# Optimization experiments

Measured on AMD Instinct MI355X. Metric: run time of the kernel, lower is better.

## Reference

```python
import jax, jax.numpy as jnp
import numpy as np


def setup_inputs() -> dict:
    key = jax.random.key(0)
    k1, k2, k3, k4, k5 = jax.random.split(key, 5)
    B, S, IN, OUT = 4, 2048, 4096, 11008
    x = jax.random.normal(k1, (B, S, IN), dtype=jnp.float32)
    # uint8-style codes stored as int32 (per-channel int8 WOQ)
    qweight = jax.random.randint(k2, (OUT, IN), 0, 256, dtype=jnp.int32)
    scales = jax.random.uniform(k3, (OUT,), dtype=jnp.float32) * 0.01 + 1e-4
    zero_points = jax.random.uniform(k4, (OUT,), dtype=jnp.float32) * 255.0
    bias = jax.random.normal(k5, (OUT,), dtype=jnp.float32)
    return {"x": x, "qweight": qweight, "scales": scales,
            "zero_points": zero_points, "bias": bias}


def reference(x, qweight, scales, zero_points, bias):
    # Inline dequantization of per-output-channel quantized weight:
    # W[o, i] = (q[o, i] - zp[o]) * scale[o]
    w = (qweight.astype(jnp.float32) - zero_points[:, None]) * scales[:, None]
    # Y = x @ W^T + b  -> [B, S, OUT]
    y = jnp.einsum("bsi,oi->bso", x, w) + bias
    return y
```

## Files before the change

kernel.cpp:

```cpp
#include <hip/hip_runtime.h>
#include <stdint.h>

#define MDIM 8192
#define NDIM 11008
#define KDIM 4096
#define BM 128
#define BN 128
#define BK 32

typedef __bf16 bf16x8 __attribute__((ext_vector_type(8)));
typedef float floatx4 __attribute__((ext_vector_type(4)));

typedef const __attribute__((address_space(1))) void* gas_ptr;
typedef __attribute__((address_space(3))) void* las_ptr;

__device__ __forceinline__ unsigned short f32_bf16_rne(float f) {
    union { float f; unsigned u; } v; v.f = f;
    unsigned r = 0x7FFFu + ((v.u >> 16) & 1u);
    return (unsigned short)((v.u + r) >> 16);
}

__global__ __launch_bounds__(256) void convert_x_kernel(
    const float* __restrict__ x, unsigned short* __restrict__ xb)
{
    const size_t gid = (size_t)blockIdx.x * 256 + threadIdx.x;
    const float4* p = (const float4*)x + gid * 2;
    float4 a = p[0], b = p[1];
    unsigned short t[8];
    t[0] = f32_bf16_rne(a.x); t[1] = f32_bf16_rne(a.y);
    t[2] = f32_bf16_rne(a.z); t[3] = f32_bf16_rne(a.w);
    t[4] = f32_bf16_rne(b.x); t[5] = f32_bf16_rne(b.y);
    t[6] = f32_bf16_rne(b.z); t[7] = f32_bf16_rne(b.w);
    *(uint4*)(xb + gid * 8) = *(const uint4*)t;
}

__global__ __launch_bounds__(256) void dequant_w_kernel(
    const int* __restrict__ q, const float* __restrict__ scales,
    const float* __restrict__ zps, unsigned short* __restrict__ wb)
{
    const size_t gid = (size_t)blockIdx.x * 256 + threadIdx.x;
    const int o = (int)(gid >> 9);
    const float s = scales[o], z = zps[o];
    const int4* p = (const int4*)q + gid * 2;
    int4 a = p[0], b = p[1];
    unsigned short t[8];
    t[0] = f32_bf16_rne(((float)a.x - z) * s);
    t[1] = f32_bf16_rne(((float)a.y - z) * s);
    t[2] = f32_bf16_rne(((float)a.z - z) * s);
    t[3] = f32_bf16_rne(((float)a.w - z) * s);
    t[4] = f32_bf16_rne(((float)b.x - z) * s);
    t[5] = f32_bf16_rne(((float)b.y - z) * s);
    t[6] = f32_bf16_rne(((float)b.z - z) * s);
    t[7] = f32_bf16_rne(((float)b.w - z) * s);
    *(uint4*)(wb + gid * 8) = *(const uint4*)t;
}

__global__ __launch_bounds__(256) void gemm_bf16_kernel(
    const unsigned short* __restrict__ A,
    const unsigned short* __restrict__ B,
    const float* __restrict__ bias,
    float* __restrict__ C)
{
    __shared__ __align__(16) unsigned short As[BM * BK];
    __shared__ __align__(16) unsigned short Bs[BN * BK];

    const int tid  = threadIdx.x;
    const int lane = tid & 63;
    const int wave = tid >> 6;
    const int wm   = (wave >> 1) * 64;
    const int wn   = (wave & 1) * 64;
    const int bm   = blockIdx.x * BM;
    const int bn   = blockIdx.y * BN;

    floatx4 acc[4][4];
#pragma unroll
    for (int i = 0; i < 4; ++i)
#pragma unroll
        for (int j = 0; j < 4; ++j)
            acc[i][j] = (floatx4){0.f, 0.f, 0.f, 0.f};

    const int mrow = lane & 15;
    const int kc   = lane >> 4;
    const int ks   = ((kc ^ (mrow & 3)) * 8);

    const int c0 = tid, c1 = tid + 256;
    const int r0 = c0 >> 2, k0c = (((c0 & 3) ^ (r0 & 3)) * 8);
    const int r1 = c1 >> 2, k1c = (((c1 & 3) ^ (r1 & 3)) * 8);
    const unsigned short* gA0 = A + (size_t)(bm + r0) * KDIM + k0c;
    const unsigned short* gA1 = A + (size_t)(bm + r1) * KDIM + k1c;
    const unsigned short* gB0 = B + (size_t)(bn + r0) * KDIM + k0c;
    const unsigned short* gB1 = B + (size_t)(bn + r1) * KDIM + k1c;
    unsigned short* lA0 = As + (wave * 64) * 8;
    unsigned short* lA1 = As + (256 + wave * 64) * 8;
    unsigned short* lB0 = Bs + (wave * 64) * 8;
    unsigned short* lB1 = Bs + (256 + wave * 64) * 8;

    for (int kt = 0; kt < KDIM; kt += BK) {
        __builtin_amdgcn_global_load_lds((gas_ptr)(gA0 + kt), (las_ptr)lA0, 16, 0, 0);
        __builtin_amdgcn_global_load_lds((gas_ptr)(gA1 + kt), (las_ptr)lA1, 16, 0, 0);
        __builtin_amdgcn_global_load_lds((gas_ptr)(gB0 + kt), (las_ptr)lB0, 16, 0, 0);
        __builtin_amdgcn_global_load_lds((gas_ptr)(gB1 + kt), (las_ptr)lB1, 16, 0, 0);
        __syncthreads();

        bf16x8 af[4], bfr[4];
#pragma unroll
        for (int i = 0; i < 4; ++i)
            af[i] = *(const bf16x8*)(As + (wm + i * 16 + mrow) * BK + ks);
#pragma unroll
        for (int j = 0; j < 4; ++j)
            bfr[j] = *(const bf16x8*)(Bs + (wn + j * 16 + mrow) * BK + ks);
#pragma unroll
        for (int i = 0; i < 4; ++i)
#pragma unroll
            for (int j = 0; j < 4; ++j)
                acc[i][j] = __builtin_amdgcn_mfma_f32_16x16x32_bf16(
                    af[i], bfr[j], acc[i][j], 0, 0, 0);
        __syncthreads();
    }

#pragma unroll
    for (int j = 0; j < 4; ++j) {
        const int col = bn + wn + j * 16 + mrow;
        const float bv = bias[col];
#pragma unroll
        for (int i = 0; i < 4; ++i) {
            const int rbase = bm + wm + i * 16 + (lane >> 4) * 4;
#pragma unroll
            for (int r = 0; r < 4; ++r)
                C[(size_t)(rbase + r) * NDIM + col] = acc[i][j][r] + bv;
        }
    }
}

__global__ __launch_bounds__(256) void gemm_fused_fallback(
    const float* __restrict__ X, const int* __restrict__ Q,
    const float* __restrict__ scales, const float* __restrict__ zps,
    const float* __restrict__ bias, float* __restrict__ C)
{
    __shared__ __align__(16) unsigned short As[BM * BK];
    __shared__ __align__(16) unsigned short Bs[BN * BK];

    const int tid  = threadIdx.x;
    const int lane = tid & 63;
    const int wave = tid >> 6;
    const int wm   = (wave >> 1) * 64;
    const int wn   = (wave & 1) * 64;
    const int bm   = blockIdx.x * BM;
    const int bn   = blockIdx.y * BN;

    floatx4 acc[4][4];
#pragma unroll
    for (int i = 0; i < 4; ++i)
#pragma unroll
        for (int j = 0; j < 4; ++j)
            acc[i][j] = (floatx4){0.f, 0.f, 0.f, 0.f};

    const int mrow = lane & 15;
    const int kq   = (lane >> 4) * 8;

    for (int kt = 0; kt < KDIM; kt += BK) {
#pragma unroll
        for (int s4 = 0; s4 < 4; ++s4) {
            const int c = tid + 256 * s4;
            const int row = c >> 3, kcb = (c & 7) * 4;
            float4 xv = *(const float4*)(X + (size_t)(bm + row) * KDIM + kt + kcb);
            unsigned short ta[4];
            ta[0] = f32_bf16_rne(xv.x); ta[1] = f32_bf16_rne(xv.y);
            ta[2] = f32_bf16_rne(xv.z); ta[3] = f32_bf16_rne(xv.w);
            *(uint2*)(As + row * BK + kcb) = *(const uint2*)ta;

            int4 qv = *(const int4*)(Q + (size_t)(bn + row) * KDIM + kt + kcb);
            const float sc = scales[bn + row], z = zps[bn + row];
            unsigned short tb[4];
            tb[0] = f32_bf16_rne(((float)qv.x - z) * sc);
            tb[1] = f32_bf16_rne(((float)qv.y - z) * sc);
            tb[2] = f32_bf16_rne(((float)qv.z - z) * sc);
            tb[3] = f32_bf16_rne(((float)qv.w - z) * sc);
            *(uint2*)(Bs + row * BK + kcb) = *(const uint2*)tb;
        }
        __syncthreads();

        bf16x8 af[4], bfr[4];
#pragma unroll
        for (int i = 0; i < 4; ++i)
            af[i] = *(const bf16x8*)(As + (wm + i * 16 + mrow) * BK + kq);
#pragma unroll
        for (int j = 0; j < 4; ++j)
            bfr[j] = *(const bf16x8*)(Bs + (wn + j * 16 + mrow) * BK + kq);
#pragma unroll
        for (int i = 0; i < 4; ++i)
#pragma unroll
            for (int j = 0; j < 4; ++j)
                acc[i][j] = __builtin_amdgcn_mfma_f32_16x16x32_bf16(
                    af[i], bfr[j], acc[i][j], 0, 0, 0);
        __syncthreads();
    }

#pragma unroll
    for (int j = 0; j < 4; ++j) {
        const int col = bn + wn + j * 16 + mrow;
        const float bv = bias[col];
#pragma unroll
        for (int i = 0; i < 4; ++i) {
            const int rbase = bm + wm + i * 16 + (lane >> 4) * 4;
#pragma unroll
            for (int r = 0; r < 4; ++r)
                C[(size_t)(rbase + r) * NDIM + col] = acc[i][j][r] + bv;
        }
    }
}

extern "C" void kernel_launch(void* const* d_in, const int* in_sizes, int n_in,
                              void* d_out, int out_size, void* d_ws, size_t ws_size,
                              hipStream_t stream) {
    const float* x  = (const float*)d_in[0];
    const int*   qw = (const int*)d_in[1];
    const float* sc = (const float*)d_in[2];
    const float* zp = (const float*)d_in[3];
    const float* bs = (const float*)d_in[4];
    float* out = (float*)d_out;

    const size_t needA = (size_t)MDIM * KDIM * sizeof(unsigned short);
    const size_t needW = (size_t)NDIM * KDIM * sizeof(unsigned short);
    dim3 grid(MDIM / BM, NDIM / BN);

    if (ws_size >= needA + needW) {
        unsigned short* xb = (unsigned short*)d_ws;
        unsigned short* wb = (unsigned short*)((char*)d_ws + needA);
        convert_x_kernel<<<dim3(MDIM * KDIM / (8 * 256)), dim3(256), 0, stream>>>(x, xb);
        dequant_w_kernel<<<dim3(NDIM * KDIM / (8 * 256)), dim3(256), 0, stream>>>(qw, sc, zp, wb);
        gemm_bf16_kernel<<<grid, dim3(256), 0, stream>>>(xb, wb, bs, out);
    } else {
        gemm_fused_fallback<<<grid, dim3(256), 0, stream>>>(x, qw, sc, zp, bs, out);
    }
}
```

Baseline: 1.410 ms.

## Replace bf16 GEMM with 256x256-tile, 4-stage LDS-pipelined, 512-thread kernel

Replaces the 128x128 single-buffered GEMM with a 256x256 tile kernel using 8 waves and a 4-deep ring of LDS buffers filled by global_load_lds prefetches three k-steps ahead. MFMA work is split into two halves interleaved with the async loads and barriers, and s_setprio raises priority during MFMA bursts. A remapped 1D grid groups tiles for L2 reuse, and output stores become nontemporal. The aim is to hide global-load latency and raise arithmetic intensity, at the cost of 128KB dynamic LDS, a larger register footprint and more barriers per k-step.

New measurement: 1.379 ms. -2.2%, faster.

```diff
diff --git a/kernel.cpp b/kernel.cpp
--- a/kernel.cpp
+++ b/kernel.cpp
@@ -55,79 +55,128 @@
     *(uint4*)(wb + gid * 8) = *(const uint4*)t;
 }
 
-__global__ __launch_bounds__(256) void gemm_bf16_kernel(
+__device__ __forceinline__ void wg_barrier() {
+    asm volatile("" ::: "memory");
+    __builtin_amdgcn_s_barrier();
+    asm volatile("" ::: "memory");
+}
+
+__global__ __launch_bounds__(512, 2) void gemm_bf16_pipe(
     const unsigned short* __restrict__ A,
     const unsigned short* __restrict__ B,
     const float* __restrict__ bias,
     float* __restrict__ C)
 {
-    __shared__ __align__(16) unsigned short As[BM * BK];
-    __shared__ __align__(16) unsigned short Bs[BN * BK];
+    extern __shared__ unsigned short lds[];
 
     const int tid  = threadIdx.x;
     const int lane = tid & 63;
     const int wave = tid >> 6;
-    const int wm   = (wave >> 1) * 64;
-    const int wn   = (wave & 1) * 64;
-    const int bm   = blockIdx.x * BM;
-    const int bn   = blockIdx.y * BN;
-
-    floatx4 acc[4][4];
-#pragma unroll
-    for (int i = 0; i < 4; ++i)
+    const int wm   = (wave >> 2) * 128;
+    const int wn   = (wave & 3) * 64;
+
+    const int wg = blockIdx.x;
+    const int f  = (wg & 7) * 172 + (wg >> 3);
+    const int mt = f & 31;
+    const int nt = f >> 5;
+    const size_t bm = (size_t)mt * 256;
+    const size_t bn = (size_t)nt * 256;
+
+    const int mrow = lane & 15;
+    const int kc   = lane >> 4;
+    const int gsw  = (mrow >> 1) & 3;
+    const int ksw  = (kc ^ gsw) * 8;
+    const int offA = (wm + mrow) * 32 + ksw;
+    const int offB = 8192 + (wn + mrow) * 32 + ksw;
+
+    const int u0 = tid, u1 = tid + 512;
+    const int r0 = u0 >> 2, c0 = (u0 & 3) ^ ((r0 >> 1) & 3);
+    const int r1 = u1 >> 2, c1 = (u1 & 3) ^ ((r1 >> 1) & 3);
+    const unsigned short* gA0 = A + (bm + r0) * KDIM + c0 * 8;
+    const unsigned short* gA1 = A + (bm + r1) * KDIM + c1 * 8;
+    const unsigned short* gB0 = B + (bn + r0) * KDIM + c0 * 8;
+    const unsigned short* gB1 = B + (bn + r1) * KDIM + c1 * 8;
+    const int dA0 = wave * 512, dA1 = 4096 + wave * 512;
+    const int dB0 = 8192 + wave * 512, dB1 = 12288 + wave * 512;
+
+    floatx4 acc[8][4];
+#pragma unroll
+    for (int i = 0; i < 8; ++i)
 #pragma unroll
         for (int j = 0; j < 4; ++j)
             acc[i][j] = (floatx4){0.f, 0.f, 0.f, 0.f};
 
-    const int mrow = lane & 15;
-    const int kc   = lane >> 4;
-    const int ks   = ((kc ^ (mrow & 3)) * 8);
-
-    const int c0 = tid, c1 = tid + 256;
-    const int r0 = c0 >> 2, k0c = (((c0 & 3) ^ (r0 & 3)) * 8);
-    const int r1 = c1 >> 2, k1c = (((c1 & 3) ^ (r1 & 3)) * 8);
-    const unsigned short* gA0 = A + (size_t)(bm + r0) * KDIM + k0c;
-    const unsigned short* gA1 = A + (size_t)(bm + r1) * KDIM + k1c;
-    const unsigned short* gB0 = B + (size_t)(bn + r0) * KDIM + k0c;
-    const unsigned short* gB1 = B + (size_t)(bn + r1) * KDIM + k1c;
-    unsigned short* lA0 = As + (wave * 64) * 8;
-    unsigned short* lA1 = As + (256 + wave * 64) * 8;
-    unsigned short* lB0 = Bs + (wave * 64) * 8;
-    unsigned short* lB1 = Bs + (256 + wave * 64) * 8;
-
-    for (int kt = 0; kt < KDIM; kt += BK) {
-        __builtin_amdgcn_global_load_lds((gas_ptr)(gA0 + kt), (las_ptr)lA0, 16, 0, 0);
-        __builtin_amdgcn_global_load_lds((gas_ptr)(gA1 + kt), (las_ptr)lA1, 16, 0, 0);
-        __builtin_amdgcn_global_load_lds((gas_ptr)(gB0 + kt), (las_ptr)lB0, 16, 0, 0);
-        __builtin_amdgcn_global_load_lds((gas_ptr)(gB1 + kt), (las_ptr)lB1, 16, 0, 0);
-        __syncthreads();
-
-        bf16x8 af[4], bfr[4];
-#pragma unroll
-        for (int i = 0; i < 4; ++i)
-            af[i] = *(const bf16x8*)(As + (wm + i * 16 + mrow) * BK + ks);
-#pragma unroll
-        for (int j = 0; j < 4; ++j)
-            bfr[j] = *(const bf16x8*)(Bs + (wn + j * 16 + mrow) * BK + ks);
-#pragma unroll
-        for (int i = 0; i < 4; ++i)
+#pragma unroll
+    for (int tt = 0; tt < 3; ++tt) {
+        unsigned short* sp = lds + tt * 16384;
+        const int ko = tt * 32;
+        __builtin_amdgcn_global_load_lds((gas_ptr)(gA0 + ko), (las_ptr)(sp + dA0), 16, 0, 0);
+        __builtin_amdgcn_global_load_lds((gas_ptr)(gA1 + ko), (las_ptr)(sp + dA1), 16, 0, 0);
+        __builtin_amdgcn_global_load_lds((gas_ptr)(gB0 + ko), (las_ptr)(sp + dB0), 16, 0, 0);
+        __builtin_amdgcn_global_load_lds((gas_ptr)(gB1 + ko), (las_ptr)(sp + dB1), 16, 0, 0);
+    }
+    asm volatile("s_waitcnt vmcnt(8)" ::: "memory");
+    wg_barrier();
+
+    for (int tb = 0; tb < 128; tb += 4) {
+#pragma unroll
+        for (int q = 0; q < 4; ++q) {
+            const int t = tb + q;
+            const unsigned short* bp = lds + q * 16384;
+            unsigned short* sp = lds + ((q + 3) & 3) * 16384;
+            int pre = t + 3; if (pre > 127) pre = 127;
+            const int ko = pre * 32;
+
+            bf16x8 af[8], bfr[4];
+#pragma unroll
+            for (int i = 0; i < 4; ++i)
+                af[i] = *(const bf16x8*)(bp + offA + i * 512);
 #pragma unroll
             for (int j = 0; j < 4; ++j)
-                acc[i][j] = __builtin_amdgcn_mfma_f32_16x16x32_bf16(
-                    af[i], bfr[j], acc[i][j], 0, 0, 0);
-        __syncthreads();
-    }
+                bfr[j] = *(const bf16x8*)(bp + offB + j * 512);
+            __builtin_amdgcn_global_load_lds((gas_ptr)(gA0 + ko), (las_ptr)(sp + dA0), 16, 0, 0);
+            __builtin_amdgcn_global_load_lds((gas_ptr)(gA1 + ko), (las_ptr)(sp + dA1), 16, 0, 0);
+            wg_barrier();
+            __builtin_amdgcn_s_setprio(1);
+#pragma unroll
+            for (int i = 0; i < 4; ++i)
+#pragma unroll
+                for (int j = 0; j < 4; ++j)
+                    acc[i][j] = __builtin_amdgcn_mfma_f32_16x16x32_bf16(
+                        af[i], bfr[j], acc[i][j], 0, 0, 0);
+            __builtin_amdgcn_s_setprio(0);
+            wg_barrier();
+#pragma unroll
+            for (int i = 4; i < 8; ++i)
+                af[i] = *(const bf16x8*)(bp + offA + i * 512);
+            __builtin_amdgcn_global_load_lds((gas_ptr)(gB0 + ko), (las_ptr)(sp + dB0), 16, 0, 0);
+            __builtin_amdgcn_global_load_lds((gas_ptr)(gB1 + ko), (las_ptr)(sp + dB1), 16, 0, 0);
+            asm volatile("s_waitcnt vmcnt(8)" ::: "memory");
+            wg_barrier();
+            __builtin_amdgcn_s_setprio(1);
+#pragma unroll
+            for (int i = 4; i < 8; ++i)
+#pragma unroll
+                for (int j = 0; j < 4; ++j)
+                    acc[i][j] = __builtin_amdgcn_mfma_f32_16x16x32_bf16(
+                        af[i], bfr[j], acc[i][j], 0, 0, 0);
+            __builtin_amdgcn_s_setprio(0);
+            wg_barrier();
+        }
+    }
+    asm volatile("s_waitcnt vmcnt(0)" ::: "memory");
 
 #pragma unroll
     for (int j = 0; j < 4; ++j) {
-        const int col = bn + wn + j * 16 + mrow;
+        const int col = (int)bn + wn + j * 16 + mrow;
         const float bv = bias[col];
 #pragma unroll
-        for (int i = 0; i < 4; ++i) {
-            const int rbase = bm + wm + i * 16 + (lane >> 4) * 4;
+        for (int i = 0; i < 8; ++i) {
+            const size_t rbase = bm + wm + i * 16 + (lane >> 4) * 4;
 #pragma unroll
             for (int r = 0; r < 4; ++r)
-                C[(size_t)(rbase + r) * NDIM + col] = acc[i][j][r] + bv;
+                __builtin_nontemporal_store(acc[i][j][r] + bv,
+                                            &C[(rbase + r) * NDIM + col]);
         }
     }
 }
@@ -222,15 +271,22 @@
 
     const size_t needA = (size_t)MDIM * KDIM * sizeof(unsigned short);
     const size_t needW = (size_t)NDIM * KDIM * sizeof(unsigned short);
-    dim3 grid(MDIM / BM, NDIM / BN);
 
     if (ws_size >= needA + needW) {
+        static bool attr_set = false;
+        if (!attr_set) {
+            hipFuncSetAttribute(reinterpret_cast<const void*>(gemm_bf16_pipe),
+                                hipFuncAttributeMaxDynamicSharedMemorySize, 131072);
+            attr_set = true;
+        }
         unsigned short* xb = (unsigned short*)d_ws;
         unsigned short* wb = (unsigned short*)((char*)d_ws + needA);
         convert_x_kernel<<<dim3(MDIM * KDIM / (8 * 256)), dim3(256), 0, stream>>>(x, xb);
         dequant_w_kernel<<<dim3(NDIM * KDIM / (8 * 256)), dim3(256), 0, stream>>>(qw, sc, zp, wb);
-        gemm_bf16_kernel<<<grid, dim3(256), 0, stream>>>(xb, wb, bs, out);
+        gemm_bf16_pipe<<<dim3((MDIM / 256) * (NDIM / 256)), dim3(512), 131072, stream>>>(
+            xb, wb, bs, out);
     } else {
+        dim3 grid(MDIM / BM, NDIM / BN);
         gemm_fused_fallback<<<grid, dim3(256), 0, stream>>>(x, qw, sc, zp, bs, out);
     }
 }
```
